# Performance work log

Hardware: AMD Instinct MI355X
Metric: run time of the kernel (lower is better)

The kernel has to match this reference:

```python
import jax, jax.numpy as jnp
import numpy as np

NUM_CLASSES = 19
COUNT = 6
EPS = 1e-5


def setup_inputs() -> dict:
    key = jax.random.key(0)
    k1, k2 = jax.random.split(key)
    x = jax.random.normal(k1, (4, 256, 256, 256), dtype=jnp.float32)  # [B, C, H, W]
    y = jax.random.randint(k2, (4, 256, 256), 0, NUM_CLASSES)          # [B, H, W]
    return {"x": x, "y": y}


def reference(x, y):
    # Faithful vectorized version of the per-class masked mean/std loop:
    # means[b,k,c] = mean of x[b,c] over pixels with y[b]==k   (if count>COUNT else 0)
    # stds[b,k,c]  = unbiased std over those pixels + eps      (if count>COUNT else 0)
    B, C, H, W = x.shape
    N = H * W
    xf = x.reshape(B, C, N)                     # [B, C, N]
    yf = y.reshape(B, N)                        # [B, N]
    # one-hot segment membership; labels like 255 simply match no class
    onehot = (yf[:, None, :] == jnp.arange(NUM_CLASSES)[None, :, None]).astype(x.dtype)  # [B, K, N]
    cnt = onehot.sum(-1)                        # [B, K]
    s = jnp.einsum('bkn,bcn->bkc', onehot, xf)          # per-class sum
    ss = jnp.einsum('bkn,bcn->bkc', onehot, xf * xf)    # per-class sum of squares
    valid = cnt > COUNT                         # [B, K]
    vm = valid[..., None]                       # [B, K, 1]
    cnt_safe = jnp.maximum(cnt, 1.0)[..., None]
    mean = s / cnt_safe
    # unbiased variance: (sum(x^2) - n*mean^2) / (n-1)
    denom = jnp.maximum(cnt - 1.0, 1.0)[..., None]
    var = jnp.maximum((ss - cnt[..., None] * mean * mean) / denom, 0.0)
    std = jnp.sqrt(jnp.where(vm, var, 1.0)) + EPS
    means = jnp.where(vm, mean, 0.0)
    stds = jnp.where(vm, std, 0.0)
    return means, stds, valid
```

## Files before the change

kernel.cpp:

```cpp
#include <hip/hip_runtime.h>

#define NCLS 19
#define NCH 256
#define NPIX 65536
#define NBATCH 4
#define TPB 256
#define EPSV 1e-5f
#define CNT_THRESH 6

__global__ __launch_bounds__(TPB) void moment_kernel(const float* __restrict__ x,
                                                     const int* __restrict__ y,
                                                     float* __restrict__ out) {
    const int tid  = threadIdx.x;
    const int lane = tid & 63;
    const int w    = tid >> 6;
    const int c = blockIdx.x;
    const int b = blockIdx.y;

    float s[NCLS], q[NCLS];
    int cnt[NCLS];
    #pragma unroll
    for (int k = 0; k < NCLS; ++k) { s[k] = 0.f; q[k] = 0.f; cnt[k] = 0; }

    const float4* xp = (const float4*)(x + ((size_t)(b * NCH + c)) * NPIX);
    const int4*   yp = (const int4*)(y + (size_t)b * NPIX);

    for (int it = tid; it < NPIX / 4; it += TPB) {
        float4 v = xp[it];
        int4   l = yp[it];
        #pragma unroll
        for (int k = 0; k < NCLS; ++k) {
            bool m0 = (l.x == k); float t0 = m0 ? v.x : 0.f;
            bool m1 = (l.y == k); float t1 = m1 ? v.y : 0.f;
            bool m2 = (l.z == k); float t2 = m2 ? v.z : 0.f;
            bool m3 = (l.w == k); float t3 = m3 ? v.w : 0.f;
            s[k] += t0; q[k] = fmaf(t0, t0, q[k]);
            s[k] += t1; q[k] = fmaf(t1, t1, q[k]);
            s[k] += t2; q[k] = fmaf(t2, t2, q[k]);
            s[k] += t3; q[k] = fmaf(t3, t3, q[k]);
            cnt[k] += (int)__popcll(__ballot(m0)) + (int)__popcll(__ballot(m1))
                    + (int)__popcll(__ballot(m2)) + (int)__popcll(__ballot(m3));
        }
    }

    __shared__ float red_s[4][NCLS];
    __shared__ float red_q[4][NCLS];
    __shared__ int   red_n[4][NCLS];
    #pragma unroll
    for (int k = 0; k < NCLS; ++k) {
        float sv = s[k], qv = q[k];
        for (int off = 32; off > 0; off >>= 1) {
            sv += __shfl_down(sv, off);
            qv += __shfl_down(qv, off);
        }
        if (lane == 0) { red_s[w][k] = sv; red_q[w][k] = qv; red_n[w][k] = cnt[k]; }
    }
    __syncthreads();

    if (tid < NCLS) {
        const int k = tid;
        float sv = 0.f, qv = 0.f; int n = 0;
        #pragma unroll
        for (int i = 0; i < 4; ++i) { sv += red_s[i][k]; qv += red_q[i][k]; n += red_n[i][k]; }
        const float nf = (float)n;
        const bool valid = n > CNT_THRESH;
        float mean = sv / fmaxf(nf, 1.0f);
        float var  = fmaxf((qv - nf * mean * mean) / fmaxf(nf - 1.0f, 1.0f), 0.0f);
        const int o = (b * NCLS + k) * NCH + c;
        out[o] = valid ? mean : 0.0f;
        out[NBATCH * NCLS * NCH + o] = valid ? (sqrtf(var) + EPSV) : 0.0f;
        if (c == 0)
            out[2 * NBATCH * NCLS * NCH + b * NCLS + k] = valid ? 1.0f : 0.0f;
    }
}

extern "C" void kernel_launch(void* const* d_in, const int* in_sizes, int n_in,
                              void* d_out, int out_size, void* d_ws, size_t ws_size,
                              hipStream_t stream) {
    const float* x = (const float*)d_in[0];
    const int*   y = (const int*)d_in[1];
    float* out = (float*)d_out;

    dim3 grid(NCH, NBATCH);
    moment_kernel<<<grid, TPB, 0, stream>>>(x, y, out);
}
```

Baseline: 427.1 us.

## Split class counting into separate kernel and process two channels per block with packed FP32

Class counts are moved out of the main loop into a small count kernel that writes per-segment partial counts to workspace, removing the per-class ballot/popcount work from every channel. The moment kernel now handles two channels per block, reusing each label load for both, and accumulates sums and squares with packed v_pk_add/v_pk_fma instructions via inline asm. This targets the ALU-bound inner loop at the cost of one extra kernel launch, double the accumulator registers (which may reduce occupancy), and half as many blocks.

```diff
diff --git a/kernel.cpp b/kernel.cpp
--- a/kernel.cpp
+++ b/kernel.cpp
@@ -7,69 +7,116 @@
 #define TPB 256
 #define EPSV 1e-5f
 #define CNT_THRESH 6
+#define CSEG 16
+#define SEGPIX (NPIX / CSEG)
+
+typedef float v2f __attribute__((ext_vector_type(2)));
+
+__global__ __launch_bounds__(TPB) void count_kernel(const int* __restrict__ y,
+                                                    int* __restrict__ part) {
+    const int b = blockIdx.x >> 4, seg = blockIdx.x & 15;
+    const int tid = threadIdx.x, lane = tid & 63, w = tid >> 6;
+    const int4* yp = (const int4*)(y + (size_t)b * NPIX + seg * SEGPIX);
+    int r[NCLS];
+    #pragma unroll
+    for (int k = 0; k < NCLS; ++k) r[k] = 0;
+    #pragma unroll
+    for (int j = 0; j < 4; ++j) {
+        int4 l = yp[j * TPB + tid];
+        #pragma unroll
+        for (int k = 0; k < NCLS; ++k)
+            r[k] += (l.x == k) + (l.y == k) + (l.z == k) + (l.w == k);
+    }
+    __shared__ int red[4][NCLS];
+    #pragma unroll
+    for (int k = 0; k < NCLS; ++k) {
+        int v = r[k];
+        for (int off = 32; off > 0; off >>= 1) v += __shfl_down(v, off);
+        if (lane == 0) red[w][k] = v;
+    }
+    __syncthreads();
+    if (tid < NCLS)
+        part[blockIdx.x * NCLS + tid] =
+            red[0][tid] + red[1][tid] + red[2][tid] + red[3][tid];
+}
 
 __global__ __launch_bounds__(TPB) void moment_kernel(const float* __restrict__ x,
                                                      const int* __restrict__ y,
+                                                     const int* __restrict__ part,
                                                      float* __restrict__ out) {
-    const int tid  = threadIdx.x;
-    const int lane = tid & 63;
-    const int w    = tid >> 6;
-    const int c = blockIdx.x;
-    const int b = blockIdx.y;
+    const int tid = threadIdx.x, lane = tid & 63, w = tid >> 6;
+    const int cp = blockIdx.x;
+    const int b  = blockIdx.y;
 
-    float s[NCLS], q[NCLS];
-    int cnt[NCLS];
+    v2f s2[NCLS], q2[NCLS];
     #pragma unroll
-    for (int k = 0; k < NCLS; ++k) { s[k] = 0.f; q[k] = 0.f; cnt[k] = 0; }
+    for (int k = 0; k < NCLS; ++k) { s2[k] = (v2f)0.f; q2[k] = (v2f)0.f; }
 
-    const float4* xp = (const float4*)(x + ((size_t)(b * NCH + c)) * NPIX);
+    const float4* xa = (const float4*)(x + ((size_t)(b * NCH + 2 * cp)) * NPIX);
+    const float4* xb = xa + NPIX / 4;
     const int4*   yp = (const int4*)(y + (size_t)b * NPIX);
 
     for (int it = tid; it < NPIX / 4; it += TPB) {
-        float4 v = xp[it];
-        int4   l = yp[it];
+        float4 va = xa[it];
+        float4 vb = xb[it];
+        int4   l  = yp[it];
         #pragma unroll
         for (int k = 0; k < NCLS; ++k) {
-            bool m0 = (l.x == k); float t0 = m0 ? v.x : 0.f;
-            bool m1 = (l.y == k); float t1 = m1 ? v.y : 0.f;
-            bool m2 = (l.z == k); float t2 = m2 ? v.z : 0.f;
-            bool m3 = (l.w == k); float t3 = m3 ? v.w : 0.f;
-            s[k] += t0; q[k] = fmaf(t0, t0, q[k]);
-            s[k] += t1; q[k] = fmaf(t1, t1, q[k]);
-            s[k] += t2; q[k] = fmaf(t2, t2, q[k]);
-            s[k] += t3; q[k] = fmaf(t3, t3, q[k]);
-            cnt[k] += (int)__popcll(__ballot(m0)) + (int)__popcll(__ballot(m1))
-                    + (int)__popcll(__ballot(m2)) + (int)__popcll(__ballot(m3));
+            v2f t;
+            bool m;
+            m = (l.x == k); t.x = m ? va.x : 0.f; t.y = m ? vb.x : 0.f;
+            asm("v_pk_add_f32 %0, %0, %1" : "+v"(s2[k]) : "v"(t));
+            asm("v_pk_fma_f32 %0, %1, %1, %0" : "+v"(q2[k]) : "v"(t));
+            m = (l.y == k); t.x = m ? va.y : 0.f; t.y = m ? vb.y : 0.f;
+            asm("v_pk_add_f32 %0, %0, %1" : "+v"(s2[k]) : "v"(t));
+            asm("v_pk_fma_f32 %0, %1, %1, %0" : "+v"(q2[k]) : "v"(t));
+            m = (l.z == k); t.x = m ? va.z : 0.f; t.y = m ? vb.z : 0.f;
+            asm("v_pk_add_f32 %0, %0, %1" : "+v"(s2[k]) : "v"(t));
+            asm("v_pk_fma_f32 %0, %1, %1, %0" : "+v"(q2[k]) : "v"(t));
+            m = (l.w == k); t.x = m ? va.w : 0.f; t.y = m ? vb.w : 0.f;
+            asm("v_pk_add_f32 %0, %0, %1" : "+v"(s2[k]) : "v"(t));
+            asm("v_pk_fma_f32 %0, %1, %1, %0" : "+v"(q2[k]) : "v"(t));
         }
     }
 
-    __shared__ float red_s[4][NCLS];
-    __shared__ float red_q[4][NCLS];
-    __shared__ int   red_n[4][NCLS];
+    __shared__ float red[4][NCLS][4];
     #pragma unroll
     for (int k = 0; k < NCLS; ++k) {
-        float sv = s[k], qv = q[k];
+        float sa = s2[k].x, sb = s2[k].y, qa = q2[k].x, qb = q2[k].y;
         for (int off = 32; off > 0; off >>= 1) {
-            sv += __shfl_down(sv, off);
-            qv += __shfl_down(qv, off);
+            sa += __shfl_down(sa, off);
+            sb += __shfl_down(sb, off);
+            qa += __shfl_down(qa, off);
+            qb += __shfl_down(qb, off);
         }
-        if (lane == 0) { red_s[w][k] = sv; red_q[w][k] = qv; red_n[w][k] = cnt[k]; }
+        if (lane == 0) { red[w][k][0] = sa; red[w][k][1] = sb; red[w][k][2] = qa; red[w][k][3] = qb; }
     }
     __syncthreads();
 
     if (tid < NCLS) {
         const int k = tid;
-        float sv = 0.f, qv = 0.f; int n = 0;
+        float sa = 0.f, sb = 0.f, qa = 0.f, qb = 0.f;
         #pragma unroll
-        for (int i = 0; i < 4; ++i) { sv += red_s[i][k]; qv += red_q[i][k]; n += red_n[i][k]; }
+        for (int i = 0; i < 4; ++i) {
+            sa += red[i][k][0]; sb += red[i][k][1];
+            qa += red[i][k][2]; qb += red[i][k][3];
+        }
+        int n = 0;
+        #pragma unroll
+        for (int i = 0; i < CSEG; ++i) n += part[(b * CSEG + i) * NCLS + k];
         const float nf = (float)n;
         const bool valid = n > CNT_THRESH;
-        float mean = sv / fmaxf(nf, 1.0f);
-        float var  = fmaxf((qv - nf * mean * mean) / fmaxf(nf - 1.0f, 1.0f), 0.0f);
-        const int o = (b * NCLS + k) * NCH + c;
-        out[o] = valid ? mean : 0.0f;
-        out[NBATCH * NCLS * NCH + o] = valid ? (sqrtf(var) + EPSV) : 0.0f;
-        if (c == 0)
+        const float inv  = 1.0f / fmaxf(nf, 1.0f);
+        const float dinv = 1.0f / fmaxf(nf - 1.0f, 1.0f);
+        float mean_a = sa * inv, mean_b = sb * inv;
+        float var_a = fmaxf((qa - nf * mean_a * mean_a) * dinv, 0.0f);
+        float var_b = fmaxf((qb - nf * mean_b * mean_b) * dinv, 0.0f);
+        const int oa = (b * NCLS + k) * NCH + 2 * cp;
+        out[oa]     = valid ? mean_a : 0.0f;
+        out[oa + 1] = valid ? mean_b : 0.0f;
+        out[NBATCH * NCLS * NCH + oa]     = valid ? (sqrtf(var_a) + EPSV) : 0.0f;
+        out[NBATCH * NCLS * NCH + oa + 1] = valid ? (sqrtf(var_b) + EPSV) : 0.0f;
+        if (cp == 0)
             out[2 * NBATCH * NCLS * NCH + b * NCLS + k] = valid ? 1.0f : 0.0f;
     }
 }
@@ -80,7 +127,10 @@
     const float* x = (const float*)d_in[0];
     const int*   y = (const int*)d_in[1];
     float* out = (float*)d_out;
+    int* part = (int*)d_ws;
 
-    dim3 grid(NCH, NBATCH);
-    moment_kernel<<<grid, TPB, 0, stream>>>(x, y, out);
+    count_kernel<<<NBATCH * CSEG, TPB, 0, stream>>>(y, part);
+
+    dim3 grid(NCH / 2, NBATCH);
+    moment_kernel<<<grid, TPB, 0, stream>>>(x, y, part, out);
 }
```

Result: faster. 402.9 us (-5.7%).
